# Optimization experiments

Measured on AMD Instinct MI355X. Metric: run time of the kernel, lower is better.

Reference implementation:

```python
import jax, jax.numpy as jnp
import numpy as np
from jax import lax

B0, H0, W0, C0, NH0 = 8, 128, 128, 192, 6
SPLIT = (8, 16)
BN_EPS = 1e-5


def setup_inputs() -> dict:
    key = jax.random.key(0)
    ks = jax.random.split(key, 32)
    r = lambda i, shape, s=0.02: jax.random.normal(ks[i], shape, dtype=jnp.float32) * s
    C, C8 = C0, C0 // 8
    L = H0 * W0
    return dict(
        x=jax.random.normal(ks[0], (B0, L, C), dtype=jnp.float32),
        w_qkv=r(1, (C, 3 * C)), b_qkv=r(2, (3 * C,)),
        w_dw1=r(3, (C, 1, 3, 3), 0.1), b_dw1=r(4, (C,)),
        g_bn1=1.0 + r(5, (C,)), be_bn1=r(6, (C,)),
        w_si1=r(7, (C8, C), 0.05), b_si1=r(8, (C8,)),
        g_si=1.0 + r(9, (C8,)), be_si=r(10, (C8,)),
        w_si2=r(11, (1, C8), 0.05), b_si2=r(12, (1,)),
        w_ci1=r(13, (C8, C), 0.05), b_ci1=r(14, (C8,)),
        g_ci=1.0 + r(15, (C8,)), be_ci=r(16, (C8,)),
        w_ci2=r(17, (C, C8), 0.05), b_ci2=r(18, (C,)),
        w_dw2=r(19, (C, 1, 3, 3), 0.1), b_dw2=r(20, (C,)),
        g_bn2=1.0 + r(21, (C,)), be_bn2=r(22, (C,)),
        w_proj=r(23, (C, C)), b_proj=r(24, (C,)),
        H=H0, W=W0,
    )


def _bn(x, g, b):  # eval-mode BatchNorm2d, running_mean=0, running_var=1, NCHW
    return x * (g / jnp.sqrt(1.0 + BN_EPS))[:, None, None] + b[:, None, None]


def _gelu(x):
    return jax.nn.gelu(x, approximate=False)  # torch nn.GELU default (erf)


def _dwconv3x3(x, w, b):  # x:(B,C,H,W), w:(C,1,3,3) depthwise
    y = lax.conv_general_dilated(x, w, (1, 1), 'SAME',
                                 feature_group_count=x.shape[1],
                                 dimension_numbers=('NCHW', 'OIHW', 'NCHW'))
    return y + b[:, None, None]


def _c1x1(x, w, b):  # 1x1 conv, w:(O,C)
    return jnp.einsum('bchw,oc->bohw', x, w) + b[:, None, None]


def _win_attn(q, k, v, H, W, Hs, Ws, nh):
    # q,k,v: (B, H*W, Cb). qkv1==qkv2==qkv3 in the source (same Linear on same x),
    # so attn1+attn2+attn3 == 3*attn1 and v1+v2+v3 == 3*v1 (faithful math).
    B, L, Cb = q.shape
    hd = Cb // nh
    scale = hd ** (-0.5)
    T = Hs * Ws

    def to_win(t):  # (B,L,Cb) -> (nW, nh, T, hd)
        t = t.reshape(B, H // Hs, Hs, W // Ws, Ws, Cb)
        t = t.transpose(0, 1, 3, 2, 4, 5).reshape(-1, T, nh, hd)
        return t.transpose(0, 2, 1, 3)

    qw, kw, vw = to_win(q), to_win(k), to_win(v)
    attn = jnp.einsum('wntd,wnsd->wnts', qw, kw) * (3.0 * scale)
    attn = jax.nn.softmax(attn, axis=-1)
    out = jnp.einsum('wnts,wnsd->wntd', attn, 3.0 * vw)  # (nW, nh, T, hd)
    out = out.transpose(0, 2, 1, 3).reshape(-1, T, Cb)
    out = out.reshape(B, H // Hs, W // Ws, Hs, Ws, Cb)
    out = out.transpose(0, 1, 3, 2, 4, 5).reshape(B, H, W, Cb)
    return out


def _forward(x, w_qkv, b_qkv, w_dw1, b_dw1, g_bn1, be_bn1,
             w_si1, b_si1, g_si, be_si, w_si2, b_si2,
             w_ci1, b_ci1, g_ci, be_ci, w_ci2, b_ci2,
             w_dw2, b_dw2, g_bn2, be_bn2, w_proj, b_proj, H, W):
    B, L, C = x.shape
    Ch = C // 2
    nh = NH0 // 2

    qkv = (x @ w_qkv + b_qkv).reshape(B, L, 3, C).transpose(2, 0, 1, 3)  # (3,B,L,C)
    mx = max(SPLIT)
    pad_b = (mx - H % mx) % mx
    pad_r = (mx - W % mx) % mx
    qi = qkv.reshape(3 * B, H, W, C)
    qi = jnp.pad(qi, ((0, 0), (0, pad_b), (0, pad_r), (0, 0)))
    _H, _W = H + pad_b, W + pad_r
    qkv = qi.reshape(3, B, _H * _W, C)
    q, k, v = qkv[0], qkv[1], qkv[2]

    fu1 = _win_attn(q[..., :Ch], k[..., :Ch], v[..., :Ch], _H, _W, SPLIT[0], SPLIT[1], nh)
    fu2 = _win_attn(q[..., Ch:], k[..., Ch:], v[..., Ch:], _H, _W, SPLIT[1], SPLIT[0], nh)
    fu = jnp.concatenate([fu1[:, :H, :W, :].reshape(B, L, Ch),
                          fu2[:, :H, :W, :].reshape(B, L, Ch)], axis=-1)

    # NOTE: the source does x.reshape(B,C,L) (a raw reshape, NOT a transpose) -- replicated.
    x_img = x.reshape(B, C, H, W)
    conv_x1 = _gelu(_bn(_dwconv3x3(x_img, w_dw1, b_dw1), g_bn1, be_bn1))

    s = _c1x1(conv_x1, w_si1, b_si1)
    s = _c1x1(_gelu(_bn(s, g_si, be_si)), w_si2, b_si2)   # (B,1,H,W)
    spatial_map = s.reshape(B, L, 1)

    c = conv_x1.mean(axis=(2, 3), keepdims=True)           # AdaptiveAvgPool2d(1)
    c = _c1x1(c, w_ci1, b_ci1)
    c = _c1x1(_gelu(_bn(c, g_ci, be_ci)), w_ci2, b_ci2)    # (B,C,1,1)
    channel_map = c.reshape(B, 1, C)

    fu = fu + fu * jax.nn.sigmoid(spatial_map)
    fu_img = jnp.swapaxes(fu, -2, -1).reshape(B, C, H, W)
    fu_img = _gelu(_bn(_dwconv3x3(fu_img, w_dw2, b_dw2), g_bn2, be_bn2))
    fu = fu_img.transpose(0, 2, 3, 1).reshape(B, L, C)
    fu = fu + fu * jax.nn.sigmoid(channel_map)
    return fu @ w_proj + b_proj


def reference(x, w_qkv, b_qkv, w_dw1, b_dw1, g_bn1, be_bn1,
              w_si1, b_si1, g_si, be_si, w_si2, b_si2,
              w_ci1, b_ci1, g_ci, be_ci, w_ci2, b_ci2,
              w_dw2, b_dw2, g_bn2, be_bn2, w_proj, b_proj, H, W):
    return _forward(x, w_qkv, b_qkv, w_dw1, b_dw1, g_bn1, be_bn1,
                    w_si1, b_si1, g_si, be_si, w_si2, b_si2,
                    w_ci1, b_ci1, g_ci, be_ci, w_ci2, b_ci2,
                    w_dw2, b_dw2, g_bn2, be_bn2, w_proj, b_proj, H, W)
```

## Files before the change

### kernel.cpp

```cpp
#include <hip/hip_runtime.h>

#define Bn 8
#define Hn 128
#define Wn 128
#define Cn 192
#define Ln (Hn*Wn)
#define Mn (Bn*Ln)
#define FUn ((size_t)Mn*Cn)
#define BANKn ((size_t)Mn*96)
#define BN_RSQ 0.9999950000374997f

typedef unsigned short ushort_t;
typedef __attribute__((ext_vector_type(8))) short short8;
typedef __attribute__((ext_vector_type(4))) float f32x4;
typedef __attribute__((ext_vector_type(4))) unsigned int uint4v;

static __device__ __forceinline__ float gelu_f(float x) {
    return 0.5f * x * (1.0f + erff(x * 0.7071067811865475f));
}
static __device__ __forceinline__ float gate1p(float x) {
    return 1.0f + 1.0f / (1.0f + __expf(-x));
}
static __device__ __forceinline__ unsigned short f2bf(float f) {
    unsigned u = __float_as_uint(f);
    return (unsigned short)((u + 0x7FFFu + ((u >> 16) & 1u)) >> 16);
}
static __device__ __forceinline__ unsigned int pk2(float lo, float hi) {
    return (unsigned int)f2bf(lo) | ((unsigned int)f2bf(hi) << 16);
}
static __device__ __forceinline__ float bf2f(ushort_t u) {
    return __uint_as_float((unsigned)u << 16);
}

__global__ __launch_bounds__(256) void qkv_mfma(const ushort_t* __restrict__ Ab,
        const float* __restrict__ Bw, const float* __restrict__ bias,
        ushort_t* __restrict__ Qp, ushort_t* __restrict__ Kp,
        ushort_t* __restrict__ Vp)
{
    __shared__ __align__(16) ushort_t smem[128 * 64 + 96 * 64];
    ushort_t* As = smem;
    ushort_t* Bs = smem + 128 * 64;
    ushort_t* St = smem;
    ushort_t* Stv = smem;
    const int br = blockIdx.y & 1;
    const int partp = blockIdx.y >> 1;
    const int wid = blockIdx.x;
    const int b = wid >> 7, win = wid & 127;
    const int n0g = partp * 192 + br * 96;
    ushort_t* dst = partp == 0 ? Qp : (partp == 1 ? Kp : Vp);
    ushort_t* bptr = dst + (br ? BANKn : 0);
    int hb, wb;
    if (br == 0) { hb = (win >> 3) * 8;  wb = (win & 7) * 16; }
    else         { hb = (win >> 4) * 16; wb = (win & 15) * 8; }
    const int tid = threadIdx.x;
    const int lane = tid & 63;
    const int wrow = (tid >> 6) * 32;
    const int r0 = lane >> 4, cl = lane & 15;
    f32x4 acc[2][6] = {};

    for (int ks = 0; ks < 3; ++ks) {
        const int k0 = ks * 64;
        if (ks) __syncthreads();
        #pragma unroll
        for (int i = 0; i < 2; ++i) {
            int s = tid + i * 256;
            int row = s >> 2, q = s & 3;
            int l = (br == 0) ? (hb + (row >> 4)) * Wn + wb + (row & 15)
                              : (hb + (row >> 3)) * Wn + wb + (row & 7);
            const ushort_t* src = Ab + (size_t)(b * Ln + l) * 192 + k0 + q * 16;
            uint4 u0 = *(const uint4*)(src);
            uint4 u1 = *(const uint4*)(src + 8);
            int r7 = row & 7;
            *(uint4*)&As[row * 64 + (((q * 2) ^ r7) * 8)] = u0;
            *(uint4*)&As[row * 64 + (((q * 2 + 1) ^ r7) * 8)] = u1;
        }
        #pragma unroll
        for (int i = 0; i < 3; ++i) {
            int f = tid + i * 256;
            int col = f % 96, kslot = f / 96;
            uint4v wv;
            #pragma unroll
            for (int e2 = 0; e2 < 4; ++e2) {
                float lo = Bw[(size_t)(k0 + kslot * 8 + 2 * e2)     * 576 + n0g + col];
                float hi = Bw[(size_t)(k0 + kslot * 8 + 2 * e2 + 1) * 576 + n0g + col];
                wv[e2] = pk2(lo, hi);
            }
            *(uint4v*)&Bs[col * 64 + ((kslot ^ (col & 7)) * 8)] = wv;
        }
        __syncthreads();
        #pragma unroll
        for (int kk = 0; kk < 2; ++kk) {
            int kslot = kk * 4 + r0;
            int ra0 = wrow + cl, ra1 = wrow + 16 + cl;
            short8 a0 = *(const short8*)&As[ra0 * 64 + ((kslot ^ (ra0 & 7)) * 8)];
            short8 a1 = *(const short8*)&As[ra1 * 64 + ((kslot ^ (ra1 & 7)) * 8)];
            #pragma unroll
            for (int n = 0; n < 6; ++n) {
                int col = n * 16 + cl;
                short8 bn = *(const short8*)&Bs[col * 64 + ((kslot ^ (col & 7)) * 8)];
                acc[0][n] = __builtin_amdgcn_mfma_f32_16x16x32_bf16(a0, bn, acc[0][n], 0, 0, 0);
                acc[1][n] = __builtin_amdgcn_mfma_f32_16x16x32_bf16(a1, bn, acc[1][n], 0, 0, 0);
            }
        }
    }
    float bv[6];
    #pragma unroll
    for (int n = 0; n < 6; ++n) bv[n] = bias[n0g + n * 16 + cl];
    __syncthreads();
    const size_t hbase = (size_t)wid * 3;
    if (partp < 2) {
        #pragma unroll
        for (int m = 0; m < 2; ++m)
            #pragma unroll
            for (int n = 0; n < 6; ++n)
                #pragma unroll
                for (int j = 0; j < 4; ++j) {
                    int t = wrow + m * 16 + r0 * 4 + j;
                    St[t * 104 + n * 16 + cl] = f2bf(acc[m][n][j] + bv[n]);
                }
        __syncthreads();
        #pragma unroll
        for (int i = 0; i < 6; ++i) {
            int f = tid + i * 256;
            int ch8 = f & 3, t = (f >> 2) & 127, hd = f >> 9;
            uint4 v = *(const uint4*)&St[t * 104 + hd * 32 + ch8 * 8];
            *(uint4*)(bptr + (hbase + hd) * 4096 + t * 32 + ch8 * 8) = v;
        }
    } else {
        #pragma unroll
        for (int m = 0; m < 2; ++m)
            #pragma unroll
            for (int n = 0; n < 6; ++n)
                #pragma unroll
                for (int j = 0; j < 4; ++j) {
                    int t = wrow + m * 16 + r0 * 4 + j;
                    Stv[(n * 16 + cl) * 136 + t] = f2bf(acc[m][n][j] + bv[n]);
                }
        __syncthreads();
        #pragma unroll
        for (int i = 0; i < 6; ++i) {
            int f = tid + i * 256;
            int t16 = f & 15, ch = (f >> 4) & 31, hd = f >> 9;
            uint4 v = *(const uint4*)&Stv[(hd * 32 + ch) * 136 + t16 * 8];
            *(uint4*)(bptr + (hbase + hd) * 4096 + ch * 128 + t16 * 8) = v;
        }
    }
}

__global__ __launch_bounds__(256) void proj_mfma(const ushort_t* __restrict__ Ab,
        const float* __restrict__ Bw, const float* __restrict__ bias,
        float* __restrict__ Cout)
{
    __shared__ __align__(16) ushort_t As[128 * 64];
    __shared__ __align__(16) ushort_t Bs[96 * 64];
    const int m0 = blockIdx.x * 128;
    const int n0 = blockIdx.y * 96;
    const int tid = threadIdx.x;
    const int lane = tid & 63;
    const int wrow = (tid >> 6) * 32;
    const int r0 = lane >> 4, cl = lane & 15;
    f32x4 acc[2][6] = {};

    for (int ks = 0; ks < 3; ++ks) {
        const int k0 = ks * 64;
        if (ks) __syncthreads();
        #pragma unroll
        for (int i = 0; i < 2; ++i) {
            int s = tid + i * 256;
            int row = s >> 2, q = s & 3;
            const ushort_t* src = Ab + (size_t)(m0 + row) * 192 + k0 + q * 16;
            uint4 u0 = *(const uint4*)(src);
            uint4 u1 = *(const uint4*)(src + 8);
            int r7 = row & 7;
            *(uint4*)&As[row * 64 + (((q * 2) ^ r7) * 8)] = u0;
            *(uint4*)&As[row * 64 + (((q * 2 + 1) ^ r7) * 8)] = u1;
        }
        #pragma unroll
        for (int i = 0; i < 3; ++i) {
            int f = tid + i * 256;
            int col = f % 96, kslot = f / 96;
            uint4v wv;
            #pragma unroll
            for (int e2 = 0; e2 < 4; ++e2) {
                float lo = Bw[(size_t)(k0 + kslot * 8 + 2 * e2)     * 192 + n0 + col];
                float hi = Bw[(size_t)(k0 + kslot * 8 + 2 * e2 + 1) * 192 + n0 + col];
                wv[e2] = pk2(lo, hi);
            }
            *(uint4v*)&Bs[col * 64 + ((kslot ^ (col & 7)) * 8)] = wv;
        }
        __syncthreads();
        #pragma unroll
        for (int kk = 0; kk < 2; ++kk) {
            int kslot = kk * 4 + r0;
            int ra0 = wrow + cl, ra1 = wrow + 16 + cl;
            short8 a0 = *(const short8*)&As[ra0 * 64 + ((kslot ^ (ra0 & 7)) * 8)];
            short8 a1 = *(const short8*)&As[ra1 * 64 + ((kslot ^ (ra1 & 7)) * 8)];
            #pragma unroll
            for (int n = 0; n < 6; ++n) {
                int col = n * 16 + cl;
                short8 bn = *(const short8*)&Bs[col * 64 + ((kslot ^ (col & 7)) * 8)];
                acc[0][n] = __builtin_amdgcn_mfma_f32_16x16x32_bf16(a0, bn, acc[0][n], 0, 0, 0);
                acc[1][n] = __builtin_amdgcn_mfma_f32_16x16x32_bf16(a1, bn, acc[1][n], 0, 0, 0);
            }
        }
    }
    #pragma unroll
    for (int m = 0; m < 2; ++m) {
        #pragma unroll
        for (int n = 0; n < 6; ++n) {
            int col = n0 + n * 16 + cl;
            float bv = bias[col];
            #pragma unroll
            for (int j = 0; j < 4; ++j) {
                int row = m0 + wrow + m * 16 + r0 * 4 + j;
                Cout[(size_t)row * 192 + col] = acc[m][n][j] + bv;
            }
        }
    }
}

__global__ __launch_bounds__(256) void attn_mfma(const ushort_t* __restrict__ Qp,
        const ushort_t* __restrict__ Kp, const ushort_t* __restrict__ Vp,
        const float* __restrict__ gate_s, ushort_t* __restrict__ fu_b)
{
    const int widx = threadIdx.x >> 6;
    const int idx = blockIdx.x * 4 + widx;
    const int jhalf = idx & 1;
    const int sub0 = idx >> 1;
    const int branch = (sub0 >= 3072) ? 1 : 0;
    const int sub = sub0 - branch * 3072;
    const int head = sub >> 10;
    const int b = (sub >> 7) & 7;
    const int win = sub & 127;
    const int L = threadIdx.x & 63;
    const int g = L >> 4, q = L & 15;
    int hb, wb;
    if (branch == 0) { hb = (win >> 3) * 8;  wb = (win & 7) * 16; }
    else             { hb = (win >> 4) * 16; wb = (win & 15) * 8; }
    const int cf = branch * 96 + head * 32;
    const int jbase = jhalf * 4;

    const size_t base = (branch ? BANKn : 0)
                      + ((size_t)(b * 128 + win) * 3 + head) * 4096;
    const ushort_t* Qw = Qp + base;
    const ushort_t* Kw = Kp + base;
    const ushort_t* Vw = Vp + base;

    short8 kf[8], qf[4];
    #pragma unroll
    for (int i = 0; i < 8; ++i)
        kf[i] = *(const short8*)(Kw + (16 * i + q) * 32 + 8 * g);
    #pragma unroll
    for (int jj = 0; jj < 4; ++jj)
        qf[jj] = *(const short8*)(Qw + (16 * (jbase + jj) + q) * 32 + 8 * g);
    short8 vf[2][4];
    #pragma unroll
    for (int dblk = 0; dblk < 2; ++dblk)
        #pragma unroll
        for (int s = 0; s < 4; ++s)
            vf[dblk][s] = *(const short8*)(Vw + (16 * dblk + q) * 128 + 32 * s + 8 * g);

    const float SC = 0.5303300858899106f;
    const int src0 = q + ((g & 1) << 5);
    const bool thi = (g >> 1) != 0;
    const bool glo = (g < 2);
    #pragma unroll
    for (int jj = 0; jj < 4; ++jj) {
        const int j = jbase + jj;
        unsigned wA[8], wB[8];
        float ss = 0.0f;
        #pragma unroll
        for (int i = 0; i < 8; ++i) {
            f32x4 z = {};
            f32x4 S = __builtin_amdgcn_mfma_f32_16x16x32_bf16(kf[i], qf[jj], z, 0, 0, 0);
            float p0 = __expf(S[0] * SC), p1 = __expf(S[1] * SC);
            float p2 = __expf(S[2] * SC), p3 = __expf(S[3] * SC);
            ss += (p0 + p1) + (p2 + p3);
            wA[i] = pk2(p0, p1);
            wB[i] = pk2(p2, p3);
        }
        ss += __shfl_xor(ss, 16);
        ss += __shfl_xor(ss, 32);
        int l_own;
        if (branch == 0) l_own = (hb + j) * Wn + wb + q;
        else             l_own = (hb + 2 * j + (q >> 3)) * Wn + wb + (q & 7);
        float s_own = 3.0f * gate_s[(size_t)b * Ln + l_own] / ss;

        f32x4 O0 = {}, O1 = {};
        #pragma unroll
        for (int s = 0; s < 4; ++s) {
            unsigned a0  = (unsigned)__shfl((int)wA[2*s],     src0);
            unsigned b0  = (unsigned)__shfl((int)wB[2*s],     src0);
            unsigned a0h = (unsigned)__shfl((int)wA[2*s],     src0 + 16);
            unsigned b0h = (unsigned)__shfl((int)wB[2*s],     src0 + 16);
            unsigned a1  = (unsigned)__shfl((int)wA[2*s+1],   src0);
            unsigned b1  = (unsigned)__shfl((int)wB[2*s+1],   src0);
            unsigned a1h = (unsigned)__shfl((int)wA[2*s+1],   src0 + 16);
            unsigned b1h = (unsigned)__shfl((int)wB[2*s+1],   src0 + 16);
            uint4v B2u;
            B2u[0] = thi ? a1  : a0;
            B2u[1] = thi ? b1  : b0;
            B2u[2] = thi ? a1h : a0h;
            B2u[3] = thi ? b1h : b0h;
            short8 B2 = *(short8*)&B2u;
            O0 = __builtin_amdgcn_mfma_f32_16x16x32_bf16(vf[0][s], B2, O0, 0, 0, 0);
            O1 = __builtin_amdgcn_mfma_f32_16x16x32_bf16(vf[1][s], B2, O1, 0, 0, 0);
        }
        unsigned w0 = pk2(O0[0] * s_own, O0[1] * s_own);
        unsigned w1 = pk2(O0[2] * s_own, O0[3] * s_own);
        unsigned w2 = pk2(O1[0] * s_own, O1[1] * s_own);
        unsigned w3 = pk2(O1[2] * s_own, O1[3] * s_own);
        unsigned a0 = (unsigned)__shfl((int)w0, src0);
        unsigned a1 = (unsigned)__shfl((int)w1, src0);
        unsigned b0 = (unsigned)__shfl((int)w0, src0 + 16);
        unsigned b1 = (unsigned)__shfl((int)w1, src0 + 16);
        unsigned c0 = (unsigned)__shfl((int)w2, src0);
        unsigned c1 = (unsigned)__shfl((int)w3, src0);
        unsigned d0 = (unsigned)__shfl((int)w2, src0 + 16);
        unsigned d1 = (unsigned)__shfl((int)w3, src0 + 16);
        uint4 o = make_uint4(glo ? a0 : c0, glo ? a1 : c1,
                             glo ? b0 : d0, glo ? b1 : d1);
        *(uint4*)(fu_b + (size_t)(b * Ln + l_own) * 192 + cf + 8 * g) = o;
    }
}

__global__ __launch_bounds__(256) void conv1_k(const float* __restrict__ x,
        const float* __restrict__ wdw, const float* __restrict__ bdw,
        const float* __restrict__ g1, const float* __restrict__ be1,
        ushort_t* __restrict__ conv1b, ushort_t* __restrict__ xb,
        float* __restrict__ pooled16)
{
    int bc = blockIdx.x;
    int rg = blockIdx.y;
    int c = bc % 192;
    const float* plane = x + (size_t)bc * Ln;
    int t = threadIdx.x;
    int sx = t & 31, sy = t >> 5;
    int w0 = sx * 4, h = rg * 8 + sy;
    float wk[9];
    #pragma unroll
    for (int i = 0; i < 9; ++i) wk[i] = wdw[c * 9 + i];
    float gb = g1[c] * BN_RSQ, bb = be1[c], bd = bdw[c];

    float a[3][6];
    #pragma unroll
    for (int i = 0; i < 3; ++i) {
        int hh = h - 1 + i;
        float4 m = make_float4(0.f, 0.f, 0.f, 0.f);
        if (hh >= 0 && hh < Hn)
            m = *(const float4*)(plane + hh * Wn + w0);
        float lf = __shfl_up(m.w, 1);
        float rt = __shfl_down(m.x, 1);
        a[i][0] = sx ? lf : 0.0f;
        a[i][1] = m.x; a[i][2] = m.y; a[i][3] = m.z; a[i][4] = m.w;
        a[i][5] = (sx < 31) ? rt : 0.0f;
    }
    *(uint2*)(xb + (size_t)bc * Ln + h * Wn + w0) =
        make_uint2(pk2(a[1][1], a[1][2]), pk2(a[1][3], a[1][4]));
    float psum = 0.0f;
    float o[4];
    #pragma unroll
    for (int p = 0; p < 4; ++p) {
        float s = wk[0] * a[0][p];
        s = fmaf(wk[1], a[0][p + 1], s);
        s = fmaf(wk[2], a[0][p + 2], s);
        s = fmaf(wk[3], a[1][p],     s);
        s = fmaf(wk[4], a[1][p + 1], s);
        s = fmaf(wk[5], a[1][p + 2], s);
        s = fmaf(wk[6], a[2][p],     s);
        s = fmaf(wk[7], a[2][p + 1], s);
        s = fmaf(wk[8], a[2][p + 2], s);
        float y = gelu_f((s + bd) * gb + bb);
        psum += y;
        o[p] = y;
    }
    *(uint2*)(conv1b + (size_t)bc * Ln + h * Wn + w0) =
        make_uint2(pk2(o[0], o[1]), pk2(o[2], o[3]));
    __shared__ float red[4];
    for (int off = 32; off; off >>= 1) psum += __shfl_down(psum, off);
    if ((t & 63) == 0) red[t >> 6] = psum;
    __syncthreads();
    if (t == 0)
        pooled16[bc * 16 + rg] = red[0] + red[1] + red[2] + red[3];
}

__global__ __launch_bounds__(128) void spatial_gate_k(const ushort_t* __restrict__ conv1b,
        const float* __restrict__ ws1g, const float* __restrict__ bs1,
        const float* __restrict__ gsi, const float* __restrict__ besi,
        const float* __restrict__ ws2, const float* __restrict__ bs2,
        float* __restrict__ gate_s)
{
    int bh = blockIdx.x;
    int b = bh >> 7, h = bh & 127;
    int w = threadIdx.x;
    __shared__ float ws1T[192 * 24];
    for (int i = w; i < 192 * 24; i += 128) {
        int c = i / 24, o = i - c * 24;
        ws1T[i] = ws1g[o * 192 + c];
    }
    __syncthreads();
    float acc24[24] = {};
    const ushort_t* base = conv1b + (size_t)b * 192 * Ln + h * Wn + w;
    #pragma unroll 4
    for (int c = 0; c < 192; ++c) {
        float v = bf2f(base[(size_t)c * Ln]);
        const float4* wp = (const float4*)&ws1T[c * 24];
        #pragma unroll
        for (int o4 = 0; o4 < 6; ++o4) {
            float4 wv = wp[o4];
            acc24[o4*4+0] = fmaf(v, wv.x, acc24[o4*4+0]);
            acc24[o4*4+1] = fmaf(v, wv.y, acc24[o4*4+1]);
            acc24[o4*4+2] = fmaf(v, wv.z, acc24[o4*4+2]);
            acc24[o4*4+3] = fmaf(v, wv.w, acc24[o4*4+3]);
        }
    }
    float s2 = bs2[0];
    #pragma unroll
    for (int o = 0; o < 24; ++o)
        s2 = fmaf(gelu_f((acc24[o] + bs1[o]) * (gsi[o] * BN_RSQ) + besi[o]), ws2[o], s2);
    gate_s[(size_t)bh * 128 + w] = gate1p(s2);
}

__global__ __launch_bounds__(192) void channel_gate_k(const float* __restrict__ pooled16,
        const float* __restrict__ w1, const float* __restrict__ b1,
        const float* __restrict__ g, const float* __restrict__ be,
        const float* __restrict__ w2, const float* __restrict__ b2,
        float* __restrict__ gate_c)
{
    int b = blockIdx.x, t = threadIdx.x;
    __shared__ float pl[192];
    __shared__ float h1[24];
    int bc = b * 192 + t;
    float s = 0.0f;
    #pragma unroll
    for (int i = 0; i < 16; ++i) s += pooled16[bc * 16 + i];
    pl[t] = s * (1.0f / Ln);
    __syncthreads();
    if (t < 24) {
        float a = b1[t];
        for (int c = 0; c < 192; ++c) a = fmaf(pl[c], w1[t * 192 + c], a);
        a = a * (g[t] * BN_RSQ) + be[t];
        h1[t] = gelu_f(a);
    }
    __syncthreads();
    float a = b2[t];
    #pragma unroll
    for (int o = 0; o < 24; ++o) a = fmaf(h1[o], w2[t * 24 + o], a);
    gate_c[b * 192 + t] = gate1p(a);
}

__global__ __launch_bounds__(256) void dwconv2_k(const ushort_t* __restrict__ fu_b,
        const float* __restrict__ gate_c,
        const float* __restrict__ wdw, const float* __restrict__ bdw,
        const float* __restrict__ g2, const float* __restrict__ be2,
        ushort_t* __restrict__ out2b)
{
    int bh = blockIdx.x >> 1;
    int whalf = blockIdx.x & 1;
    int b = bh >> 7, h = bh & 127;
    int tid = threadIdx.x;
    __shared__ float cwp[24 * 105];
    for (int idx = tid; idx < 24 * 96; idx += 256) {
        int c8 = idx / 96, r = idx - c8 * 96;
        float v;
        if (r < 72) {
            int i = r / 9, p = r - i * 9;
            v = wdw[(c8 * 8 + i) * 9 + p];
        } else {
            int r2 = r - 72;
            int i = r2 / 3, j = r2 - i * 3;
            int c = c8 * 8 + i;
            float A = g2[c] * BN_RSQ;
            v = (j == 0) ? A : (j == 1) ? fmaf(bdw[c], A, be2[c])
                                        : gate_c[b * 192 + c];
        }
        cwp[c8 * 105 + r] = v;
    }
    __syncthreads();
    const size_t outrow = (size_t)(b * Ln + h * Wn) * 192;
    for (int it = 0; it < 6; ++it) {
        int item = it * 256 + tid;
        int w = whalf * 64 + item / 24;
        int c8 = item % 24;
        int co = c8 * 8;
        const float* wp = &cwp[c8 * 105];
        uint4 nb[3][3];
        #pragma unroll
        for (int r = 0; r < 3; ++r)
            #pragma unroll
            for (int d = 0; d < 3; ++d)
                nb[r][d] = make_uint4(0u, 0u, 0u, 0u);
        #pragma unroll
        for (int r = 0; r < 3; ++r) {
            int hh = h - 1 + r;
            if (hh < 0 || hh >= Hn) continue;
            const ushort_t* rp = fu_b + (size_t)(b * Ln + hh * Wn) * 192 + co;
            #pragma unroll
            for (int d = 0; d < 3; ++d) {
                int w2 = w - 1 + d;
                if (w2 < 0 || w2 >= Wn) continue;
                nb[r][d] = *(const uint4*)(rp + (size_t)w2 * 192);
            }
        }
        unsigned ou[4];
        #pragma unroll
        for (int i = 0; i < 8; ++i) {
            float s = 0.0f;
            #pragma unroll
            for (int r = 0; r < 3; ++r) {
                #pragma unroll
                for (int d = 0; d < 3; ++d) {
                    unsigned word = ((const unsigned*)&nb[r][d])[i >> 1];
                    float v = __uint_as_float((i & 1) ? (word & 0xffff0000u)
                                                      : (word << 16));
                    s = fmaf(wp[i * 9 + r * 3 + d], v, s);
                }
            }
            float A = wp[72 + i * 3];
            float Bc = wp[72 + i * 3 + 1];
            float G = wp[72 + i * 3 + 2];
            float y = gelu_f(fmaf(s, A, Bc)) * G;
            if (i & 1) ou[i >> 1] |= (unsigned)f2bf(y) << 16;
            else       ou[i >> 1] = (unsigned)f2bf(y);
        }
        *(uint4*)(out2b + outrow + (size_t)w * 192 + co) =
            make_uint4(ou[0], ou[1], ou[2], ou[3]);
    }
}

extern "C" void kernel_launch(void* const* d_in, const int* in_sizes, int n_in,
                              void* d_out, int out_size, void* d_ws, size_t ws_size,
                              hipStream_t stream) {
    (void)in_sizes; (void)n_in; (void)out_size; (void)ws_size;
    const float* x      = (const float*)d_in[0];
    const float* w_qkv  = (const float*)d_in[1];
    const float* b_qkv  = (const float*)d_in[2];
    const float* w_dw1  = (const float*)d_in[3];
    const float* b_dw1  = (const float*)d_in[4];
    const float* g_bn1  = (const float*)d_in[5];
    const float* be_bn1 = (const float*)d_in[6];
    const float* w_si1  = (const float*)d_in[7];
    const float* b_si1  = (const float*)d_in[8];
    const float* g_si   = (const float*)d_in[9];
    const float* be_si  = (const float*)d_in[10];
    const float* w_si2  = (const float*)d_in[11];
    const float* b_si2  = (const float*)d_in[12];
    const float* w_ci1  = (const float*)d_in[13];
    const float* b_ci1  = (const float*)d_in[14];
    const float* g_ci   = (const float*)d_in[15];
    const float* be_ci  = (const float*)d_in[16];
    const float* w_ci2  = (const float*)d_in[17];
    const float* b_ci2  = (const float*)d_in[18];
    const float* w_dw2  = (const float*)d_in[19];
    const float* b_dw2  = (const float*)d_in[20];
    const float* g_bn2  = (const float*)d_in[21];
    const float* be_bn2 = (const float*)d_in[22];
    const float* w_proj = (const float*)d_in[23];
    const float* b_proj = (const float*)d_in[24];

    float* ws = (float*)d_ws;
    ushort_t* conv1b = (ushort_t*)ws;
    ushort_t* Qp     = (ushort_t*)ws;
    ushort_t* Kp     = (ushort_t*)(ws + FUn / 2);
    ushort_t* out2b  = (ushort_t*)(ws + 8000000);
    float* gate_s    = ws + FUn;
    float* gate_c    = gate_s + (size_t)Bn * Ln;
    float* pooled16  = gate_c + Bn * 192;
    ushort_t* xb     = (ushort_t*)d_out;
    ushort_t* fu_b   = (ushort_t*)d_out;
    ushort_t* Vp     = (ushort_t*)d_out + FUn;

    conv1_k<<<dim3(Bn * 192, 16), 256, 0, stream>>>(x, w_dw1, b_dw1, g_bn1, be_bn1,
                                                    conv1b, xb, pooled16);
    spatial_gate_k<<<Bn * Hn, 128, 0, stream>>>(conv1b, w_si1, b_si1, g_si, be_si,
                                                w_si2, b_si2, gate_s);
    channel_gate_k<<<Bn, 192, 0, stream>>>(pooled16, w_ci1, b_ci1, g_ci, be_ci,
                                           w_ci2, b_ci2, gate_c);
    qkv_mfma<<<dim3(Bn * 128, 6), 256, 0, stream>>>(xb, w_qkv, b_qkv, Qp, Kp, Vp);
    attn_mfma<<<3072, 256, 0, stream>>>(Qp, Kp, Vp, gate_s, fu_b);
    dwconv2_k<<<Bn * Hn * 2, 256, 0, stream>>>(fu_b, gate_c,
                                               w_dw2, b_dw2, g_bn2, be_bn2, out2b);
    proj_mfma<<<dim3(Mn / 128, 2), 256, 0, stream>>>(out2b, w_proj, b_proj, (float*)d_out);
}
```

Before: 295.1 us.

## Compute Q, K and V in one block to reuse the gathered A tile

The QKV GEMM kernel now computes all three Q/K/V column groups in one block instead of launching a separate block per part, so the windowed gather of x into shared memory happens once rather than three times. The grid shrinks from 6 to 2 in y, and each block holds three accumulator sets (144 floats per thread) plus a larger weight tile in LDS. This cuts redundant global reads and address math, but raises register pressure and LDS use, which may lower occupancy. It also leaves fewer blocks in flight.

```diff
diff --git a/kernel.cpp b/kernel.cpp
--- a/kernel.cpp
+++ b/kernel.cpp
@@ -37,18 +37,13 @@
         ushort_t* __restrict__ Qp, ushort_t* __restrict__ Kp,
         ushort_t* __restrict__ Vp)
 {
-    __shared__ __align__(16) ushort_t smem[128 * 64 + 96 * 64];
-    ushort_t* As = smem;
-    ushort_t* Bs = smem + 128 * 64;
-    ushort_t* St = smem;
-    ushort_t* Stv = smem;
-    const int br = blockIdx.y & 1;
-    const int partp = blockIdx.y >> 1;
+    __shared__ __align__(16) ushort_t smem[128 * 64 + 3 * 96 * 64];
+    ushort_t* As  = smem;
+    ushort_t* Bs3 = smem + 128 * 64;
+    ushort_t* St  = smem;
     const int wid = blockIdx.x;
+    const int br  = blockIdx.y;
     const int b = wid >> 7, win = wid & 127;
-    const int n0g = partp * 192 + br * 96;
-    ushort_t* dst = partp == 0 ? Qp : (partp == 1 ? Kp : Vp);
-    ushort_t* bptr = dst + (br ? BANKn : 0);
     int hb, wb;
     if (br == 0) { hb = (win >> 3) * 8;  wb = (win & 7) * 16; }
     else         { hb = (win >> 4) * 16; wb = (win & 15) * 8; }
@@ -56,7 +51,7 @@
     const int lane = tid & 63;
     const int wrow = (tid >> 6) * 32;
     const int r0 = lane >> 4, cl = lane & 15;
-    f32x4 acc[2][6] = {};
+    f32x4 acc[3][2][6] = {};
 
     for (int ks = 0; ks < 3; ++ks) {
         const int k0 = ks * 64;
@@ -75,17 +70,19 @@
             *(uint4*)&As[row * 64 + (((q * 2 + 1) ^ r7) * 8)] = u1;
         }
         #pragma unroll
-        for (int i = 0; i < 3; ++i) {
+        for (int i = 0; i < 9; ++i) {
             int f = tid + i * 256;
-            int col = f % 96, kslot = f / 96;
+            int col288 = f % 288, kslot = f / 288;
+            int part = col288 / 96, col = col288 - part * 96;
+            int gcol = part * 192 + br * 96 + col;
             uint4v wv;
             #pragma unroll
             for (int e2 = 0; e2 < 4; ++e2) {
-                float lo = Bw[(size_t)(k0 + kslot * 8 + 2 * e2)     * 576 + n0g + col];
-                float hi = Bw[(size_t)(k0 + kslot * 8 + 2 * e2 + 1) * 576 + n0g + col];
+                float lo = Bw[(size_t)(k0 + kslot * 8 + 2 * e2)     * 576 + gcol];
+                float hi = Bw[(size_t)(k0 + kslot * 8 + 2 * e2 + 1) * 576 + gcol];
                 wv[e2] = pk2(lo, hi);
             }
-            *(uint4v*)&Bs[col * 64 + ((kslot ^ (col & 7)) * 8)] = wv;
+            *(uint4v*)&Bs3[part * 6144 + col * 64 + ((kslot ^ (col & 7)) * 8)] = wv;
         }
         __syncthreads();
         #pragma unroll
@@ -95,54 +92,64 @@
             short8 a0 = *(const short8*)&As[ra0 * 64 + ((kslot ^ (ra0 & 7)) * 8)];
             short8 a1 = *(const short8*)&As[ra1 * 64 + ((kslot ^ (ra1 & 7)) * 8)];
             #pragma unroll
-            for (int n = 0; n < 6; ++n) {
-                int col = n * 16 + cl;
-                short8 bn = *(const short8*)&Bs[col * 64 + ((kslot ^ (col & 7)) * 8)];
-                acc[0][n] = __builtin_amdgcn_mfma_f32_16x16x32_bf16(a0, bn, acc[0][n], 0, 0, 0);
-                acc[1][n] = __builtin_amdgcn_mfma_f32_16x16x32_bf16(a1, bn, acc[1][n], 0, 0, 0);
-            }
-        }
-    }
-    float bv[6];
-    #pragma unroll
-    for (int n = 0; n < 6; ++n) bv[n] = bias[n0g + n * 16 + cl];
+            for (int part = 0; part < 3; ++part) {
+                #pragma unroll
+                for (int n = 0; n < 6; ++n) {
+                    int col = n * 16 + cl;
+                    short8 bn = *(const short8*)&Bs3[part * 6144 + col * 64 +
+                                                     ((kslot ^ (col & 7)) * 8)];
+                    acc[part][0][n] = __builtin_amdgcn_mfma_f32_16x16x32_bf16(a0, bn, acc[part][0][n], 0, 0, 0);
+                    acc[part][1][n] = __builtin_amdgcn_mfma_f32_16x16x32_bf16(a1, bn, acc[part][1][n], 0, 0, 0);
+                }
+            }
+        }
+    }
+    const size_t hbase = (size_t)wid * 3;
     __syncthreads();
-    const size_t hbase = (size_t)wid * 3;
-    if (partp < 2) {
-        #pragma unroll
-        for (int m = 0; m < 2; ++m)
-            #pragma unroll
-            for (int n = 0; n < 6; ++n)
+    #pragma unroll
+    for (int part = 0; part < 3; ++part) {
+        ushort_t* dst = part == 0 ? Qp : (part == 1 ? Kp : Vp);
+        ushort_t* bptr = dst + (br ? BANKn : 0);
+        float bv[6];
+        #pragma unroll
+        for (int n = 0; n < 6; ++n) bv[n] = bias[part * 192 + br * 96 + n * 16 + cl];
+        if (part) __syncthreads();
+        if (part < 2) {
+            #pragma unroll
+            for (int m = 0; m < 2; ++m)
                 #pragma unroll
-                for (int j = 0; j < 4; ++j) {
-                    int t = wrow + m * 16 + r0 * 4 + j;
-                    St[t * 104 + n * 16 + cl] = f2bf(acc[m][n][j] + bv[n]);
-                }
-        __syncthreads();
-        #pragma unroll
-        for (int i = 0; i < 6; ++i) {
-            int f = tid + i * 256;
-            int ch8 = f & 3, t = (f >> 2) & 127, hd = f >> 9;
-            uint4 v = *(const uint4*)&St[t * 104 + hd * 32 + ch8 * 8];
-            *(uint4*)(bptr + (hbase + hd) * 4096 + t * 32 + ch8 * 8) = v;
-        }
-    } else {
-        #pragma unroll
-        for (int m = 0; m < 2; ++m)
-            #pragma unroll
-            for (int n = 0; n < 6; ++n)
+                for (int n = 0; n < 6; ++n)
+                    #pragma unroll
+                    for (int j = 0; j < 4; ++j) {
+                        int t = wrow + m * 16 + r0 * 4 + j;
+                        St[t * 104 + n * 16 + cl] = f2bf(acc[part][m][n][j] + bv[n]);
+                    }
+            __syncthreads();
+            #pragma unroll
+            for (int i = 0; i < 6; ++i) {
+                int f = tid + i * 256;
+                int ch8 = f & 3, t = (f >> 2) & 127, hd = f >> 9;
+                uint4 v = *(const uint4*)&St[t * 104 + hd * 32 + ch8 * 8];
+                *(uint4*)(bptr + (hbase + hd) * 4096 + t * 32 + ch8 * 8) = v;
+            }
+        } else {
+            #pragma unroll
+            for (int m = 0; m < 2; ++m)
                 #pragma unroll
-                for (int j = 0; j < 4; ++j) {
-                    int t = wrow + m * 16 + r0 * 4 + j;
-                    Stv[(n * 16 + cl) * 136 + t] = f2bf(acc[m][n][j] + bv[n]);
-                }
-        __syncthreads();
-        #pragma unroll
-        for (int i = 0; i < 6; ++i) {
-            int f = tid + i * 256;
-            int t16 = f & 15, ch = (f >> 4) & 31, hd = f >> 9;
-            uint4 v = *(const uint4*)&Stv[(hd * 32 + ch) * 136 + t16 * 8];
-            *(uint4*)(bptr + (hbase + hd) * 4096 + ch * 128 + t16 * 8) = v;
+                for (int n = 0; n < 6; ++n)
+                    #pragma unroll
+                    for (int j = 0; j < 4; ++j) {
+                        int t = wrow + m * 16 + r0 * 4 + j;
+                        St[(n * 16 + cl) * 136 + t] = f2bf(acc[part][m][n][j] + bv[n]);
+                    }
+            __syncthreads();
+            #pragma unroll
+            for (int i = 0; i < 6; ++i) {
+                int f = tid + i * 256;
+                int t16 = f & 15, ch = (f >> 4) & 31, hd = f >> 9;
+                uint4 v = *(const uint4*)&St[(hd * 32 + ch) * 136 + t16 * 8];
+                *(uint4*)(bptr + (hbase + hd) * 4096 + ch * 128 + t16 * 8) = v;
+            }
         }
     }
 }
@@ -576,7 +583,7 @@
                                                 w_si2, b_si2, gate_s);
     channel_gate_k<<<Bn, 192, 0, stream>>>(pooled16, w_ci1, b_ci1, g_ci, be_ci,
                                            w_ci2, b_ci2, gate_c);
-    qkv_mfma<<<dim3(Bn * 128, 6), 256, 0, stream>>>(xb, w_qkv, b_qkv, Qp, Kp, Vp);
+    qkv_mfma<<<dim3(Bn * 128, 2), 256, 0, stream>>>(xb, w_qkv, b_qkv, Qp, Kp, Vp);
     attn_mfma<<<3072, 256, 0, stream>>>(Qp, Kp, Vp, gate_s, fu_b);
     dwconv2_k<<<Bn * Hn * 2, 256, 0, stream>>>(fu_b, gate_c,
                                                w_dw2, b_dw2, g_bn2, be_bn2, out2b);
```

Measured after the change: 521.4 us. 76.7% more time.
